# Kernel optimization log

Hardware: AMD Instinct MI355X
Metric: run time of the kernel (lower is better)

The kernel has to match this reference:

```python
import jax, jax.numpy as jnp
import numpy as np
import math

B, S, H, D = 1, 2048, 12, 128
DIM = H * D
BLKQ, BLKK = 128, 64
TOPK = 0.2
EPS = 1e-6
NEG = -1e30


def setup_inputs() -> dict:
    key = jax.random.key(0)
    ks = jax.random.split(key, 8)
    hidden_states = jax.random.normal(ks[0], (B, S, DIM), jnp.float32)
    # interleaved RoPE tables: even slots hold cos, odd slots hold sin phase copies
    pos = np.arange(S, dtype=np.float64)[:, None]
    inv = 1.0 / (10000.0 ** (np.arange(0, D, 2, dtype=np.float64) / D))
    ang = pos * inv[None, :]                       # [S, D/2]
    freqs_cos = jnp.asarray(np.repeat(np.cos(ang), 2, axis=-1), jnp.float32).reshape(1, S, 1, D)
    freqs_sin = jnp.asarray(np.repeat(np.sin(ang), 2, axis=-1), jnp.float32).reshape(1, S, 1, D)
    sc = 1.0 / math.sqrt(DIM)
    Wq = jax.random.normal(ks[1], (DIM, DIM), jnp.float32) * sc
    Wk = jax.random.normal(ks[2], (DIM, DIM), jnp.float32) * sc
    Wv = jax.random.normal(ks[3], (DIM, DIM), jnp.float32) * sc
    Wo = jax.random.normal(ks[4], (DIM, DIM), jnp.float32) * sc
    bq = jax.random.normal(ks[5], (DIM,), jnp.float32) * 0.01
    bk = jax.random.normal(ks[6], (DIM,), jnp.float32) * 0.01
    bv = jax.random.normal(ks[7], (DIM,), jnp.float32) * 0.01
    bo = jnp.zeros((DIM,), jnp.float32)
    gq = jnp.ones((DIM,), jnp.float32)
    gk = jnp.ones((DIM,), jnp.float32)
    return dict(hidden_states=hidden_states, freqs_cos=freqs_cos, freqs_sin=freqs_sin,
                Wq=Wq, bq=bq, Wk=Wk, bk=bk, Wv=Wv, bv=bv, Wo=Wo, bo=bo, gq=gq, gk=gk)


def _rmsnorm(x, g):
    return x * jax.lax.rsqrt(jnp.mean(x * x, axis=-1, keepdims=True) + EPS) * g


def _rope(x, fc, fs):
    # x: [B,S,H,D]; interleaved even/odd rotation as in _apply_rotary_emb
    x1 = x[..., 0::2]
    x2 = x[..., 1::2]
    cos = fc[..., 0::2]
    sin = fs[..., 1::2]
    even = x1 * cos - x2 * sin
    odd = x1 * sin + x2 * cos
    return jnp.stack([even, odd], axis=-1).reshape(x.shape)


def _sla(q, k, v):
    # q,k,v: [B,H,S,D]. Top-k block-sparse exact attention + linear attention
    # (softmax feature map) on the unselected blocks, jointly normalized.
    nqb, nkb = S // BLKQ, S // BLKK
    ksel = max(1, int(math.ceil(TOPK * nkb)))
    qb = q.reshape(B, H, nqb, BLKQ, D).mean(axis=3)
    kb = k.reshape(B, H, nkb, BLKK, D).mean(axis=3)
    blk_scores = jnp.einsum('bhqd,bhkd->bhqk', qb, kb)
    _, idx = jax.lax.top_k(blk_scores, ksel)                  # [B,H,nqb,ksel]
    bmask = (jax.nn.one_hot(idx, nkb, dtype=jnp.float32).sum(axis=-2) > 0)
    mask = jnp.repeat(jnp.repeat(bmask, BLKQ, axis=2), BLKK, axis=3)  # [B,H,S,S]

    scale = 1.0 / math.sqrt(D)
    s = jnp.einsum('bhqd,bhkd->bhqk', q, k) * scale
    m = jnp.max(jnp.where(mask, s, NEG), axis=-1, keepdims=True)
    p = jnp.where(mask, jnp.exp(s - m), 0.0)
    num_s = jnp.einsum('bhqk,bhkd->bhqd', p, v)
    den_s = p.sum(axis=-1, keepdims=True)

    lq = jax.nn.softmax(q, axis=-1)
    lk = jax.nn.softmax(k, axis=-1)
    L = jnp.where(mask, 0.0, jnp.einsum('bhqd,bhkd->bhqk', lq, lk))
    num_l = jnp.einsum('bhqk,bhkd->bhqd', L, v)
    den_l = L.sum(axis=-1, keepdims=True)

    w = jnp.exp(-m)  # bring linear part onto the max-shifted exp scale
    return (num_s + w * num_l) / (den_s + w * den_l)


def reference(hidden_states, freqs_cos, freqs_sin, Wq, bq, Wk, bk, Wv, bv, Wo, bo, gq, gk):
    q = _rmsnorm(hidden_states @ Wq + bq, gq).reshape(B, S, H, D)
    k = _rmsnorm(hidden_states @ Wk + bk, gk).reshape(B, S, H, D)
    v = (hidden_states @ Wv + bv).reshape(B, S, H, D)
    q = _rope(q, freqs_cos, freqs_sin)
    k = _rope(k, freqs_cos, freqs_sin)
    q, k, v = (t.transpose(0, 2, 1, 3) for t in (q, k, v))  # [B,H,S,D]
    o = _sla(q, k, v)
    o = o.transpose(0, 2, 1, 3).reshape(B, S, DIM)
    return o @ Wo + bo
```

## Files before the change

### kernel.cpp

```cpp
#include <hip/hip_runtime.h>
#include <hip/hip_bf16.h>

#define SQ   2048
#define DIMM 1536
#define QS   4608
#define NH   12
#define DH   128
#define NQB  16
#define NKB  32
#define KSEL 7

typedef unsigned short u16;
typedef __bf16 bf16x8 __attribute__((ext_vector_type(8)));
typedef _Float16 f16x8 __attribute__((ext_vector_type(8)));
typedef short  s16x8  __attribute__((ext_vector_type(8)));
typedef float  f32x4  __attribute__((ext_vector_type(4)));
typedef u16    u16x4  __attribute__((ext_vector_type(4)));

__device__ __forceinline__ float bf2f(u16 u) {
  unsigned int x = ((unsigned int)u) << 16;
  return __builtin_bit_cast(float, x);
}
__device__ __forceinline__ u16 f2bf(float f) {
  unsigned int x = __builtin_bit_cast(unsigned int, f);
  x += 0x7fffu + ((x >> 16) & 1u);
  return (u16)(x >> 16);
}

typedef __attribute__((address_space(3))) void lds_vt;
typedef const __attribute__((address_space(1))) void g_vt;
__device__ __forceinline__ void dma16(const void* g, void* l) {
  __builtin_amdgcn_global_load_lds((g_vt*)g, (lds_vt*)l, 16, 0, 0);
}

__global__ __launch_bounds__(256) void prep_all(const float* __restrict__ hs,
                                                u16* __restrict__ hh,
                                                u16* __restrict__ hl,
                                                const float* __restrict__ W0,
                                                const float* __restrict__ W1,
                                                const float* __restrict__ W2,
                                                const float* __restrict__ W3,
                                                u16* __restrict__ WTh,
                                                u16* __restrict__ WTl) {
  __shared__ float tile[64][65];
  int bx = blockIdx.x;
  if (bx < 1536) {
    size_t i = ((size_t)bx * 256 + threadIdx.x) * 8;
    f32x4 a = *(const f32x4*)&hs[i];
    f32x4 b = *(const f32x4*)&hs[i + 4];
    s16x8 h, l;
    #pragma unroll
    for (int j = 0; j < 4; j++) {
      u16 hj = f2bf(a[j]); h[j] = (short)hj; l[j] = (short)f2bf(a[j] - bf2f(hj));
      u16 hk = f2bf(b[j]); h[4 + j] = (short)hk; l[4 + j] = (short)f2bf(b[j] - bf2f(hk));
    }
    *(s16x8*)&hh[i] = h;
    *(s16x8*)&hl[i] = l;
    return;
  }
  int b2 = bx - 1536;
  int wi = b2 / 576;
  int rest = b2 % 576;
  int k0 = (rest / 24) * 64, n0 = (rest % 24) * 64;
  const float* W = (wi == 0) ? W0 : (wi == 1) ? W1 : (wi == 2) ? W2 : W3;
  int x = threadIdx.x & 63, y = threadIdx.x >> 6;
  #pragma unroll
  for (int i = 0; i < 16; i++) {
    int k = y + i * 4;
    tile[k][x] = W[(size_t)(k0 + k) * DIMM + n0 + x];
  }
  __syncthreads();
  size_t obase = (size_t)wi * DIMM * DIMM;
  #pragma unroll
  for (int rep = 0; rep < 2; rep++) {
    int u = threadIdx.x + rep * 256;
    int n = u >> 3, c8 = u & 7;
    s16x8 hv, lv;
    #pragma unroll
    for (int e = 0; e < 8; e++) {
      float v = tile[c8 * 8 + e][n];
      if (wi == 3) {
        hv[e] = (short)__builtin_bit_cast(u16, (_Float16)v);
      } else {
        u16 hb = f2bf(v);
        hv[e] = (short)hb;
        lv[e] = (short)f2bf(v - bf2f(hb));
      }
    }
    size_t oi = obase + (size_t)(n0 + n) * DIMM + k0 + c8 * 8;
    *(s16x8*)&WTh[oi] = hv;
    if (wi != 3) *(s16x8*)&WTl[oi] = lv;
  }
}

__global__ __launch_bounds__(512, 4) void gemm3_k(const u16* __restrict__ Ahp,
                                                  const u16* __restrict__ Alp,
                                                  const u16* __restrict__ WTh,
                                                  const u16* __restrict__ WTl,
                                                  const float* __restrict__ bq,
                                                  const float* __restrict__ bk,
                                                  const float* __restrict__ bv,
                                                  float* __restrict__ C,
                                                  u16* __restrict__ vbfT) {
  __shared__ u16 As[2][128][64];
  __shared__ u16 Bs[2][128][64];
  const int tid = threadIdx.x;
  const int w = tid >> 6, lane = tid & 63, quad = lane >> 4, l16 = lane & 15;
  const int wr = w >> 2, wc = w & 3;
  const int m_base = blockIdx.y * 128;
  const int nt = blockIdx.x;
  const int wi = nt / 12;
  const int n_in = (nt % 12) * 128;
  const u16* Bh0 = WTh + ((size_t)wi * DIMM + n_in) * DIMM;
  const u16* Bl0 = WTl + ((size_t)wi * DIMM + n_in) * DIMM;
  const float* bias = (wi == 0) ? bq : (wi == 1) ? bk : bv;
  const bool split = (wi != 2);

  const int srow = lane >> 3;
  const int skc = (((lane & 7) ^ srow) * 8);
  const int rx = (l16 & 7);

  f32x4 zero4 = {0.f, 0.f, 0.f, 0.f};
  f32x4 acc[4][2];
  #pragma unroll
  for (int i = 0; i < 4; i++)
    #pragma unroll
    for (int j = 0; j < 2; j++) acc[i][j] = zero4;

  for (int k0 = 0; k0 < DIMM; k0 += 64) {
    #pragma unroll
    for (int c = 0; c < 2; c++) {
      int r0 = w * 16 + c * 8;
      int row = r0 + srow;
      dma16(&Ahp[(size_t)(m_base + row) * DIMM + k0 + skc], &As[0][r0][0]);
      dma16(&Bh0[(size_t)row * DIMM + k0 + skc], &Bs[0][r0][0]);
      if (split) {
        dma16(&Alp[(size_t)(m_base + row) * DIMM + k0 + skc], &As[1][r0][0]);
        dma16(&Bl0[(size_t)row * DIMM + k0 + skc], &Bs[1][r0][0]);
      }
    }
    __syncthreads();
    #pragma unroll
    for (int kk = 0; kk < 2; kk++) {
      const int coff = ((kk * 4 + quad) ^ rx) * 8;
      bf16x8 afh[4], afl[4], bfh[2], bfl[2];
      #pragma unroll
      for (int i = 0; i < 4; i++)
        afh[i] = __builtin_bit_cast(bf16x8,
                 *(const s16x8*)&As[0][wr * 64 + i * 16 + l16][coff]);
      #pragma unroll
      for (int j = 0; j < 2; j++)
        bfh[j] = __builtin_bit_cast(bf16x8,
                 *(const s16x8*)&Bs[0][wc * 32 + j * 16 + l16][coff]);
      if (split) {
        #pragma unroll
        for (int i = 0; i < 4; i++)
          afl[i] = __builtin_bit_cast(bf16x8,
                   *(const s16x8*)&As[1][wr * 64 + i * 16 + l16][coff]);
        #pragma unroll
        for (int j = 0; j < 2; j++)
          bfl[j] = __builtin_bit_cast(bf16x8,
                   *(const s16x8*)&Bs[1][wc * 32 + j * 16 + l16][coff]);
      }
      #pragma unroll
      for (int i = 0; i < 4; i++)
        #pragma unroll
        for (int j = 0; j < 2; j++) {
          acc[i][j] = __builtin_amdgcn_mfma_f32_16x16x32_bf16(afh[i], bfh[j], acc[i][j], 0, 0, 0);
          if (split) {
            acc[i][j] = __builtin_amdgcn_mfma_f32_16x16x32_bf16(afh[i], bfl[j], acc[i][j], 0, 0, 0);
            acc[i][j] = __builtin_amdgcn_mfma_f32_16x16x32_bf16(afl[i], bfh[j], acc[i][j], 0, 0, 0);
          }
        }
    }
    __syncthreads();
  }

  if (wi != 2) {
    #pragma unroll
    for (int i = 0; i < 4; i++)
      #pragma unroll
      for (int j = 0; j < 2; j++) {
        int tc = wc * 32 + j * 16 + l16;
        float bv2 = bias[n_in + tc];
        #pragma unroll
        for (int rg = 0; rg < 4; rg++) {
          int r = m_base + wr * 64 + i * 16 + quad * 4 + rg;
          C[(size_t)r * QS + nt * 128 + tc] = acc[i][j][rg] + bv2;
        }
      }
  } else {
    int hh = nt % 12;
    int bblk = blockIdx.y * 2 + wr;
    u16* vb = vbfT + (size_t)(hh * NKB + bblk) * 8192;
    int kb8 = quad >> 1;
    int klo = (quad & 1) * 4;
    #pragma unroll
    for (int i = 0; i < 4; i++) {
      int k8 = (i * 2 + kb8);
      #pragma unroll
      for (int j = 0; j < 2; j++) {
        int d = wc * 32 + j * 16 + l16;
        float bv2 = bias[n_in + d];
        u16x4 o;
        #pragma unroll
        for (int rg = 0; rg < 4; rg++) o[rg] = f2bf(acc[i][j][rg] + bv2);
        *(u16x4*)&vb[d * 64 + ((k8 ^ (d & 7)) << 3) + klo] = o;
      }
    }
  }
}

__global__ __launch_bounds__(256) void gemm_o(const u16* __restrict__ Ap,
                                              const u16* __restrict__ Bp,
                                              const float* __restrict__ bias,
                                              float* __restrict__ C) {
  __shared__ u16 As[64][64];
  __shared__ u16 Bs[128][64];
  const int tid = threadIdx.x;
  const int w = tid >> 6, lane = tid & 63, quad = lane >> 4, l16 = lane & 15;
  const int wr = w >> 1, wc = w & 1;
  const int m_base = blockIdx.y * 64, n_base = blockIdx.x * 128;
  const int srow = lane >> 3;
  const int skc = (((lane & 7) ^ srow) * 8);
  const int rx = (l16 & 7);

  f32x4 zero4 = {0.f, 0.f, 0.f, 0.f};
  f32x4 acc[2][4];
  #pragma unroll
  for (int i = 0; i < 2; i++)
    #pragma unroll
    for (int j = 0; j < 4; j++) acc[i][j] = zero4;

  for (int k0 = 0; k0 < DIMM; k0 += 64) {
    #pragma unroll
    for (int c = 0; c < 2; c++) {
      int r0 = w * 16 + c * 8;
      int row = r0 + srow;
      dma16(&Ap[(size_t)(m_base + row) * DIMM + k0 + skc], &As[r0][0]);
    }
    #pragma unroll
    for (int c = 0; c < 4; c++) {
      int r0 = w * 32 + c * 8;
      int row = r0 + srow;
      dma16(&Bp[(size_t)(n_base + row) * DIMM + k0 + skc], &Bs[r0][0]);
    }
    __syncthreads();
    #pragma unroll
    for (int kk = 0; kk < 2; kk++) {
      const int coff = ((kk * 4 + quad) ^ rx) * 8;
      f16x8 af[2], bf[4];
      #pragma unroll
      for (int i = 0; i < 2; i++)
        af[i] = __builtin_bit_cast(f16x8,
                *(const s16x8*)&As[wr * 32 + i * 16 + l16][coff]);
      #pragma unroll
      for (int j = 0; j < 4; j++)
        bf[j] = __builtin_bit_cast(f16x8,
                *(const s16x8*)&Bs[wc * 64 + j * 16 + l16][coff]);
      #pragma unroll
      for (int i = 0; i < 2; i++)
        #pragma unroll
        for (int j = 0; j < 4; j++)
          acc[i][j] = __builtin_amdgcn_mfma_f32_16x16x32_f16(af[i], bf[j], acc[i][j], 0, 0, 0);
    }
    __syncthreads();
  }
  #pragma unroll
  for (int i = 0; i < 2; i++)
    #pragma unroll
    for (int j = 0; j < 4; j++) {
      int c = n_base + wc * 64 + j * 16 + l16;
      float bv2 = bias[c];
      #pragma unroll
      for (int rg = 0; rg < 4; rg++) {
        int r = m_base + wr * 32 + i * 16 + quad * 4 + rg;
        C[(size_t)r * DIMM + c] = acc[i][j][rg] + bv2;
      }
    }
}

__global__ __launch_bounds__(256) void norm_rope_k(float* __restrict__ qkv,
                                                   const float* __restrict__ gq,
                                                   const float* __restrict__ gk,
                                                   const float* __restrict__ fc,
                                                   const float* __restrict__ fs,
                                                   u16* __restrict__ qbf,
                                                   u16* __restrict__ kbf) {
  int s = blockIdx.x;
  float* row = qkv + (size_t)s * QS + (blockIdx.y == 0 ? 0 : DIMM);
  const float* g = (blockIdx.y == 0) ? gq : gk;
  u16* obase = (blockIdx.y == 0) ? qbf : kbf;
  int t = threadIdx.x;
  float ss = 0.f;
  #pragma unroll
  for (int i = 0; i < 6; i++) {
    float v = row[t + i * 256];
    ss += v * v;
  }
  #pragma unroll
  for (int m = 1; m < 64; m <<= 1) ss += __shfl_xor(ss, m, 64);
  __shared__ float wsum[4];
  if ((t & 63) == 0) wsum[t >> 6] = ss;
  __syncthreads();
  float tot = wsum[0] + wsum[1] + wsum[2] + wsum[3];
  float sc = rsqrtf(tot / 1536.0f + 1e-6f);
  #pragma unroll
  for (int i = 0; i < 3; i++) {
    int p = t + i * 256;
    int h = p >> 6, ip = p & 63;
    int base = h * 128 + 2 * ip;
    float x1 = row[base] * sc * g[base];
    float x2 = row[base + 1] * sc * g[base + 1];
    float c = fc[(size_t)s * 128 + 2 * ip];
    float sn = fs[(size_t)s * 128 + 2 * ip + 1];
    float ev = x1 * c - x2 * sn;
    float od = x1 * sn + x2 * c;
    row[base]     = ev;
    row[base + 1] = od;
    int gsk = ip >> 2, e = (2 * ip) & 7;
    int cc = (gsk & 8) | ((gsk ^ (s & 7)) & 7);
    u16* ob = obase + ((size_t)h * SQ + s) * 128;
    unsigned int pack = (unsigned int)f2bf(ev) | ((unsigned int)f2bf(od) << 16);
    *(unsigned int*)&ob[cc * 8 + e] = pack;
  }
}

__global__ __launch_bounds__(256) void kvmeans_k(const float* __restrict__ qf,
                                                 const float* __restrict__ kf,
                                                 const u16* __restrict__ vbfT,
                                                 float* __restrict__ KV,
                                                 float* __restrict__ slk,
                                                 float* __restrict__ qb,
                                                 float* __restrict__ kb) {
  __shared__ u16 lkT[128 * 72];
  __shared__ u16 vtT[128 * 64];
  int h = blockIdx.y, t = threadIdx.x;
  if (blockIdx.x >= NKB) {
    int mx = blockIdx.x - NKB;
    if (t < 128) {
      if (mx < NQB) {
        float a = 0.f;
        for (int r = 0; r < 128; r++) a += qf[(size_t)(mx * 128 + r) * QS + h * DH + t];
        qb[(h * NQB + mx) * DH + t] = a * (1.0f / 128.0f);
      } else {
        int ki = mx - NQB;
        float a = 0.f;
        for (int r = 0; r < 64; r++) a += kf[(size_t)(ki * 64 + r) * QS + h * DH + t];
        kb[(h * NKB + ki) * DH + t] = a * (1.0f / 64.0f);
      }
    }
    return;
  }
  int kbi = blockIdx.x;
  int w = t >> 6, lane = t & 63, quad = lane >> 4, l16 = lane & 15;

  {
    const u16* vsrc = vbfT + ((size_t)(h * NKB + kbi)) * 128 * 64;
    #pragma unroll
    for (int c = 0; c < 4; c++)
      dma16(vsrc + (w * 32 + c * 8) * 64 + lane * 8, &vtT[(w * 32 + c * 8) * 64]);
  }
  {
    int r = t >> 2, q4 = t & 3;
    const float* kr = kf + (size_t)(kbi * 64 + r) * QS + h * DH;
    f32x4 x[8];
    float mx = -3.4e38f;
    #pragma unroll
    for (int i = 0; i < 8; i++) {
      x[i] = *(const f32x4*)&kr[q4 * 32 + i * 4];
      mx = fmaxf(mx, fmaxf(fmaxf(x[i][0], x[i][1]), fmaxf(x[i][2], x[i][3])));
    }
    mx = fmaxf(mx, __shfl_xor(mx, 1, 64));
    mx = fmaxf(mx, __shfl_xor(mx, 2, 64));
    float sum = 0.f;
    #pragma unroll
    for (int i = 0; i < 8; i++)
      #pragma unroll
      for (int e = 0; e < 4; e++) { float v = __expf(x[i][e] - mx); x[i][e] = v; sum += v; }
    sum += __shfl_xor(sum, 1, 64);
    sum += __shfl_xor(sum, 2, 64);
    float inv = 1.0f / sum;
    #pragma unroll
    for (int i = 0; i < 8; i++)
      #pragma unroll
      for (int e = 0; e < 4; e++)
        lkT[(q4 * 32 + i * 4 + e) * 72 + r] = f2bf(x[i][e] * inv);
  }
  __syncthreads();

  f32x4 zero4 = {0.f, 0.f, 0.f, 0.f};
  f32x4 acc[2][8];
  #pragma unroll
  for (int i = 0; i < 2; i++)
    #pragma unroll
    for (int j = 0; j < 8; j++) acc[i][j] = zero4;
  #pragma unroll
  for (int kk = 0; kk < 2; kk++) {
    bf16x8 af[2];
    #pragma unroll
    for (int i = 0; i < 2; i++)
      af[i] = __builtin_bit_cast(bf16x8,
              *(const s16x8*)&lkT[(w * 32 + i * 16 + l16) * 72 + kk * 32 + quad * 8]);
    const int voff = ((kk * 4 + quad) ^ (l16 & 7)) * 8;
    #pragma unroll
    for (int j = 0; j < 8; j++) {
      bf16x8 vb = __builtin_bit_cast(bf16x8, *(const s16x8*)&vtT[(j * 16 + l16) * 64 + voff]);
      #pragma unroll
      for (int i = 0; i < 2; i++)
        acc[i][j] = __builtin_amdgcn_mfma_f32_16x16x32_bf16(af[i], vb, acc[i][j], 0, 0, 0);
    }
  }
  float* out = KV + (size_t)(h * NKB + kbi) * 16384;
  #pragma unroll
  for (int i = 0; i < 2; i++)
    #pragma unroll
    for (int j = 0; j < 8; j++) {
      #pragma unroll
      for (int rg = 0; rg < 4; rg++) {
        int r = w * 32 + i * 16 + quad * 4 + rg;
        int c = j * 16 + l16;
        out[(size_t)r * 128 + c] = acc[i][j][rg];
      }
    }
  if (t < 128) {
    float a = 0.f;
    #pragma unroll
    for (int c8 = 0; c8 < 8; c8++) {
      s16x8 v8 = *(const s16x8*)&lkT[t * 72 + c8 * 8];
      #pragma unroll
      for (int e = 0; e < 8; e++) a += bf2f((u16)v8[e]);
    }
    slk[(h * NKB + kbi) * DH + t] = a;
  }
}

__global__ __launch_bounds__(256) void kvtot_topk_k(const float* __restrict__ KV,
                                                    const float* __restrict__ slk,
                                                    const float* __restrict__ qb,
                                                    const float* __restrict__ kb,
                                                    float* __restrict__ KVtot,
                                                    float* __restrict__ sltot,
                                                    int* __restrict__ sel) {
  int h = blockIdx.y, t = threadIdx.x;
  if (blockIdx.x < 64) {
    int e = blockIdx.x * 256 + t;
    float a = 0.f;
    for (int b = 0; b < NKB; b++) a += KV[(size_t)(h * NKB + b) * 16384 + e];
    KVtot[(size_t)h * 16384 + e] = a;
    if (blockIdx.x == 0 && t < 128) {
      float s2 = 0.f;
      for (int b = 0; b < NKB; b++) s2 += slk[(h * NKB + b) * DH + t];
      sltot[h * DH + t] = s2;
    }
    return;
  }
  int qi = blockIdx.x - 64;
  __shared__ float scs[NKB];
  int r = t >> 3, sub = t & 7;
  const float* qv = qb + (size_t)(h * NQB + qi) * DH;
  const float* kv2 = kb + (size_t)(h * NKB + r) * DH;
  float a = 0.f;
  #pragma unroll
  for (int dd = 0; dd < 16; dd++) a += qv[sub * 16 + dd] * kv2[sub * 16 + dd];
  a += __shfl_xor(a, 1, 64);
  a += __shfl_xor(a, 2, 64);
  a += __shfl_xor(a, 4, 64);
  if (sub == 0) scs[r] = a;
  __syncthreads();
  if (t == 0) {
    unsigned int used = 0;
    for (int it = 0; it < KSEL; it++) {
      float best = -3.4e38f; int bi = 0;
      for (int j = 0; j < NKB; j++)
        if (!((used >> j) & 1) && scs[j] > best) { best = scs[j]; bi = j; }
      used |= 1u << bi;
      sel[(h * NQB + qi) * 8 + it] = bi;
    }
  }
}

__global__ __launch_bounds__(256) void attn_k(const u16* __restrict__ qbf,
                                              const u16* __restrict__ kbf,
                                              const u16* __restrict__ vbfT,
                                              const int* __restrict__ sel,
                                              const float* __restrict__ KV,
                                              const float* __restrict__ slk,
                                              const float* __restrict__ KVtot,
                                              const float* __restrict__ sltot,
                                              u16* __restrict__ of16) {
  __shared__ u16 smem[25600];
  __shared__ float mrow[64], lrow[64], dent[64], slsh[128];
  __shared__ int selsh[KSEL];
  u16* qt  = smem;
  u16* vtT = smem + 8192;
  u16* kt  = smem + 16384;
  u16* ptb = smem + 16384;
  u16* MT  = smem + 8192;

  int h = blockIdx.y, qi = blockIdx.x, tid = threadIdx.x;
  int w = tid >> 6, lane = tid & 63, quad = lane >> 4, l16 = lane & 15;

  {
    const u16* qsrc = qbf + ((size_t)h * SQ + qi * 64) * 128;
    #pragma unroll
    for (int c = 0; c < 4; c++)
      dma16(qsrc + (w * 16 + c * 4) * 128 + lane * 8, &qt[(w * 16 + c * 4) * 128]);
  }
  if (tid < KSEL) selsh[tid] = sel[(h * NQB + (qi >> 1)) * 8 + tid];
  __syncthreads();

  float m_run[4], l_run[4];
  f32x4 zero4 = {0.f, 0.f, 0.f, 0.f};
  f32x4 oacc[8];
  #pragma unroll
  for (int rg = 0; rg < 4; rg++) { m_run[rg] = -3.0e38f; l_run[rg] = 0.f; }
  #pragma unroll
  for (int nt = 0; nt < 8; nt++) oacc[nt] = zero4;

  for (int bi = 0; bi < KSEL; bi++) {
    int b = selsh[bi];
    {
      const u16* ksrc = kbf + ((size_t)h * SQ + b * 64) * 128;
      #pragma unroll
      for (int c = 0; c < 4; c++)
        dma16(ksrc + (w * 16 + c * 4) * 128 + lane * 8, &kt[(w * 16 + c * 4) * 128]);
      const u16* vsrc = vbfT + ((size_t)(h * NKB + b)) * 128 * 64;
      #pragma unroll
      for (int c = 0; c < 4; c++)
        dma16(vsrc + (w * 32 + c * 8) * 64 + lane * 8, &vtT[(w * 32 + c * 8) * 64]);
    }
    __syncthreads();

    f32x4 sacc[4];
    #pragma unroll
    for (int nt = 0; nt < 4; nt++) sacc[nt] = zero4;
    __builtin_amdgcn_s_setprio(1);
    #pragma unroll
    for (int kk = 0; kk < 4; kk++) {
      const int kkq = kk * 4 + quad;
      const int qoff = ((kkq & 8) | ((kkq ^ (l16 & 7)) & 7)) * 8;
      bf16x8 af = __builtin_bit_cast(bf16x8, *(const s16x8*)&qt[(w * 16 + l16) * 128 + qoff]);
      #pragma unroll
      for (int nt = 0; nt < 4; nt++) {
        bf16x8 bfr = __builtin_bit_cast(bf16x8, *(const s16x8*)&kt[(nt * 16 + l16) * 128 + qoff]);
        sacc[nt] = __builtin_amdgcn_mfma_f32_16x16x32_bf16(af, bfr, sacc[nt], 0, 0, 0);
      }
    }
    __builtin_amdgcn_s_setprio(0);
    const float SCALE = 0.08838834764831845f;
    #pragma unroll
    for (int nt = 0; nt < 4; nt++) sacc[nt] *= SCALE;

    #pragma unroll
    for (int rg = 0; rg < 4; rg++) {
      float bmax = fmaxf(fmaxf(sacc[0][rg], sacc[1][rg]),
                         fmaxf(sacc[2][rg], sacc[3][rg]));
      bmax = fmaxf(bmax, __shfl_xor(bmax, 1, 64));
      bmax = fmaxf(bmax, __shfl_xor(bmax, 2, 64));
      bmax = fmaxf(bmax, __shfl_xor(bmax, 4, 64));
      bmax = fmaxf(bmax, __shfl_xor(bmax, 8, 64));
      float mold = m_run[rg];
      float mnew = fmaxf(mold, bmax);
      float alpha = __expf(mold - mnew);
      float rs = 0.f;
      #pragma unroll
      for (int nt = 0; nt < 4; nt++) {
        float p = __expf(sacc[nt][rg] - mnew);
        sacc[nt][rg] = p; rs += p;
      }
      rs += __shfl_xor(rs, 1, 64);
      rs += __shfl_xor(rs, 2, 64);
      rs += __shfl_xor(rs, 4, 64);
      rs += __shfl_xor(rs, 8, 64);
      m_run[rg] = mnew;
      l_run[rg] = l_run[rg] * alpha + rs;
      #pragma unroll
      for (int nt = 0; nt < 8; nt++) oacc[nt][rg] *= alpha;
    }
    __syncthreads();
    #pragma unroll
    for (int rg = 0; rg < 4; rg++) {
      int r = w * 16 + quad * 4 + rg;
      #pragma unroll
      for (int nt = 0; nt < 4; nt++) ptb[r * 72 + nt * 16 + l16] = f2bf(sacc[nt][rg]);
    }
    __syncthreads();

    __builtin_amdgcn_s_setprio(1);
    #pragma unroll
    for (int kk = 0; kk < 2; kk++) {
      bf16x8 pa = __builtin_bit_cast(bf16x8, *(const s16x8*)&ptb[(w * 16 + l16) * 72 + kk * 32 + quad * 8]);
      #pragma unroll
      for (int nt = 0; nt < 8; nt++) {
        const int voff = ((kk * 4 + quad) ^ (l16 & 7)) * 8;
        bf16x8 vb = __builtin_bit_cast(bf16x8, *(const s16x8*)&vtT[(nt * 16 + l16) * 64 + voff]);
        oacc[nt] = __builtin_amdgcn_mfma_f32_16x16x32_bf16(pa, vb, oacc[nt], 0, 0, 0);
      }
    }
    __builtin_amdgcn_s_setprio(0);
    __syncthreads();
  }

  if (l16 == 0) {
    #pragma unroll
    for (int rg = 0; rg < 4; rg++) {
      int r = w * 16 + quad * 4 + rg;
      mrow[r] = m_run[rg];
      lrow[r] = l_run[rg];
    }
  }
  if (tid < 128) {
    float a = sltot[h * DH + tid];
    #pragma unroll
    for (int i = 0; i < KSEL; i++) a -= slk[(h * NKB + selsh[i]) * DH + tid];
    slsh[tid] = a;
  }
  for (int i = 0; i < 16; i++) {
    int idx = i * 256 + tid;
    int e4 = idx * 4;
    int d1 = e4 >> 7, d2 = e4 & 127;
    f32x4 a = *(const f32x4*)&KVtot[(size_t)h * 16384 + e4];
    #pragma unroll
    for (int k2 = 0; k2 < KSEL; k2++) {
      f32x4 s4 = *(const f32x4*)&KV[(size_t)(h * NKB + selsh[k2]) * 16384 + e4];
      a -= s4;
    }
    #pragma unroll
    for (int j = 0; j < 4; j++) MT[(d2 + j) * 136 + d1] = f2bf(a[j]);
  }
  __syncthreads();

  {
    int r = tid >> 2, sub = tid & 3;
    float w_r = __expf(-mrow[r]);
    float mx = -3.4e38f;
    #pragma unroll
    for (int gi = 0; gi < 4; gi++) {
      int gc = sub * 4 + gi;
      int c = (gc & 8) | ((gc ^ (r & 7)) & 7);
      #pragma unroll
      for (int e = 0; e < 8; e++) mx = fmaxf(mx, bf2f(qt[r * 128 + c * 8 + e]));
    }
    mx = fmaxf(mx, __shfl_xor(mx, 1, 64));
    mx = fmaxf(mx, __shfl_xor(mx, 2, 64));
    float sum = 0.f;
    #pragma unroll
    for (int gi = 0; gi < 4; gi++) {
      int gc = sub * 4 + gi;
      int c = (gc & 8) | ((gc ^ (r & 7)) & 7);
      #pragma unroll
      for (int e = 0; e < 8; e++) sum += __expf(bf2f(qt[r * 128 + c * 8 + e]) - mx);
    }
    sum += __shfl_xor(sum, 1, 64);
    sum += __shfl_xor(sum, 2, 64);
    float sc2 = w_r / sum;
    float dl = 0.f;
    #pragma unroll
    for (int gi = 0; gi < 4; gi++) {
      int gc = sub * 4 + gi;
      int c = (gc & 8) | ((gc ^ (r & 7)) & 7);
      #pragma unroll
      for (int e = 0; e < 8; e++) {
        float lq = __expf(bf2f(qt[r * 128 + c * 8 + e]) - mx) * sc2;
        dl += lq * slsh[gc * 8 + e];
        qt[r * 128 + c * 8 + e] = f2bf(lq);
      }
    }
    dl += __shfl_xor(dl, 1, 64);
    dl += __shfl_xor(dl, 2, 64);
    if (sub == 0) dent[r] = lrow[r] + dl;
  }
  __syncthreads();

  __builtin_amdgcn_s_setprio(1);
  #pragma unroll
  for (int kk = 0; kk < 4; kk++) {
    const int kkq = kk * 4 + quad;
    const int qoff = ((kkq & 8) | ((kkq ^ (l16 & 7)) & 7)) * 8;
    bf16x8 af = __builtin_bit_cast(bf16x8, *(const s16x8*)&qt[(w * 16 + l16) * 128 + qoff]);
    #pragma unroll
    for (int nt = 0; nt < 8; nt++) {
      bf16x8 mb = __builtin_bit_cast(bf16x8, *(const s16x8*)&MT[(nt * 16 + l16) * 136 + kk * 32 + quad * 8]);
      oacc[nt] = __builtin_amdgcn_mfma_f32_16x16x32_bf16(af, mb, oacc[nt], 0, 0, 0);
    }
  }
  __builtin_amdgcn_s_setprio(0);

  #pragma unroll
  for (int rg = 0; rg < 4; rg++) {
    int r = w * 16 + quad * 4 + rg;
    float inv = 1.0f / dent[r];
    #pragma unroll
    for (int nt = 0; nt < 8; nt++) {
      int c = nt * 16 + l16;
      float v = oacc[nt][rg] * inv;
      size_t oi = (size_t)(qi * 64 + r) * DIMM + h * DH + c;
      of16[oi] = __builtin_bit_cast(u16, (_Float16)v);
    }
  }
}

extern "C" void kernel_launch(void* const* d_in, const int* in_sizes, int n_in,
                              void* d_out, int out_size, void* d_ws, size_t ws_size,
                              hipStream_t stream) {
  const float* hs = (const float*)d_in[0];
  const float* fc = (const float*)d_in[1];
  const float* fs = (const float*)d_in[2];
  const float* Wq = (const float*)d_in[3];
  const float* bq = (const float*)d_in[4];
  const float* Wk = (const float*)d_in[5];
  const float* bk = (const float*)d_in[6];
  const float* Wv = (const float*)d_in[7];
  const float* bv = (const float*)d_in[8];
  const float* Wo = (const float*)d_in[9];
  const float* bo = (const float*)d_in[10];
  const float* gq = (const float*)d_in[11];
  const float* gk = (const float*)d_in[12];

  char* p = (char*)d_ws;
  auto alloc = [&](size_t bytes) {
    char* r = p; p += (bytes + 255) & ~(size_t)255; return r;
  };
  u16* WTh = (u16*)alloc((size_t)4 * DIMM * DIMM * 2);
  u16* WTl = (u16*)alloc((size_t)4 * DIMM * DIMM * 2);
  u16* hsh = (u16*)alloc((size_t)SQ * DIMM * 2);
  u16* hsl = (u16*)alloc((size_t)SQ * DIMM * 2);
  float* qkv = (float*)alloc((size_t)SQ * QS * 4);
  u16* qbf = (u16*)alloc((size_t)NH * SQ * DH * 2);
  u16* kbf = (u16*)alloc((size_t)NH * SQ * DH * 2);
  u16* vbfT = (u16*)alloc((size_t)NH * NKB * DH * 64 * 2);
  float* qb = (float*)alloc((size_t)NH * NQB * DH * 4);
  float* kb = (float*)alloc((size_t)NH * NKB * DH * 4);
  int* sel = (int*)alloc((size_t)NH * NQB * 8 * 4);
  float* KV = (float*)alloc((size_t)NH * NKB * DH * DH * 4);
  float* slk = (float*)alloc((size_t)NH * NKB * DH * 4);
  float* KVtot = (float*)alloc((size_t)NH * DH * DH * 4);
  float* sltot = (float*)alloc((size_t)NH * DH * 4);

  float* qf = qkv;
  float* kf = qkv + DIMM;

  prep_all<<<1536 + 2304, 256, 0, stream>>>(hs, hsh, hsl, Wq, Wk, Wv, Wo, WTh, WTl);

  gemm3_k<<<dim3(36, 16), 512, 0, stream>>>(hsh, hsl, WTh, WTl, bq, bk, bv, qkv, vbfT);

  norm_rope_k<<<dim3(SQ, 2), 256, 0, stream>>>(qkv, gq, gk, fc, fs, qbf, kbf);
  kvmeans_k<<<dim3(NKB + NQB + NKB, NH), 256, 0, stream>>>(qf, kf, vbfT, KV, slk, qb, kb);
  kvtot_topk_k<<<dim3(64 + NQB, NH), 256, 0, stream>>>(KV, slk, qb, kb, KVtot, sltot, sel);

  u16* of16 = hsh;
  attn_k<<<dim3(2 * NQB, NH), 256, 0, stream>>>(qbf, kbf, vbfT, sel, KV, slk, KVtot, sltot, of16);

  const u16* WTo = WTh + (size_t)3 * DIMM * DIMM;
  gemm_o<<<dim3(12, 32), 256, 0, stream>>>(of16, WTo, bo, (float*)d_out);
}
```

Before: 306.8 us.

## Double-buffer QKV GEMM K-loop and precompute linear-attention MT per query block

The QKV GEMM now splits each 64-wide K step into two 32-wide halves held in separate LDS buffers, issuing the DMA for the next half while MFMAs run on the current one. This hides global load latency inside the K loop. Separately, a new mt_k kernel builds the bf16 transposed KV-minus-selected matrix once per query block and writes it pre-swizzled to global memory. attn_k then loads it with DMA instead of recomputing it, removing redundant fp32 reductions that were done twice per query block. This adds a kernel launch and extra global traffic, and reuses the hsl buffer as scratch.

```diff
diff --git a/kernel.cpp b/kernel.cpp
--- a/kernel.cpp
+++ b/kernel.cpp
@@ -102,8 +102,8 @@
                                                   const float* __restrict__ bv,
                                                   float* __restrict__ C,
                                                   u16* __restrict__ vbfT) {
-  __shared__ u16 As[2][128][64];
-  __shared__ u16 Bs[2][128][64];
+  __shared__ u16 As[2][2][128][32];
+  __shared__ u16 Bs[2][2][128][32];
   const int tid = threadIdx.x;
   const int w = tid >> 6, lane = tid & 63, quad = lane >> 4, l16 = lane & 15;
   const int wr = w >> 2, wc = w & 3;
@@ -116,9 +116,11 @@
   const float* bias = (wi == 0) ? bq : (wi == 1) ? bk : bv;
   const bool split = (wi != 2);
 
-  const int srow = lane >> 3;
-  const int skc = (((lane & 7) ^ srow) * 8);
-  const int rx = (l16 & 7);
+  const int srow = lane >> 2;
+  const int skc = (((lane & 3) ^ (srow & 3)) * 8);
+  const int r0s = w * 16;
+  const size_t aoff = (size_t)(m_base + r0s + srow) * DIMM + skc;
+  const size_t boff = (size_t)(r0s + srow) * DIMM + skc;
 
   f32x4 zero4 = {0.f, 0.f, 0.f, 0.f};
   f32x4 acc[4][2];
@@ -127,52 +129,55 @@
     #pragma unroll
     for (int j = 0; j < 2; j++) acc[i][j] = zero4;
 
-  for (int k0 = 0; k0 < DIMM; k0 += 64) {
-    #pragma unroll
-    for (int c = 0; c < 2; c++) {
-      int r0 = w * 16 + c * 8;
-      int row = r0 + srow;
-      dma16(&Ahp[(size_t)(m_base + row) * DIMM + k0 + skc], &As[0][r0][0]);
-      dma16(&Bh0[(size_t)row * DIMM + k0 + skc], &Bs[0][r0][0]);
-      if (split) {
-        dma16(&Alp[(size_t)(m_base + row) * DIMM + k0 + skc], &As[1][r0][0]);
-        dma16(&Bl0[(size_t)row * DIMM + k0 + skc], &Bs[1][r0][0]);
-      }
-    }
+  auto stage = [&](int b, int k0) {
+    dma16(&Ahp[aoff + k0], &As[b][0][r0s][0]);
+    dma16(&Bh0[boff + k0], &Bs[b][0][r0s][0]);
+    if (split) {
+      dma16(&Alp[aoff + k0], &As[b][1][r0s][0]);
+      dma16(&Bl0[boff + k0], &Bs[b][1][r0s][0]);
+    }
+  };
+  const int coff = (quad ^ (l16 & 3)) * 8;
+  auto compute = [&](int b) {
+    bf16x8 afh[4], afl[4], bfh[2], bfl[2];
+    #pragma unroll
+    for (int i = 0; i < 4; i++)
+      afh[i] = __builtin_bit_cast(bf16x8,
+               *(const s16x8*)&As[b][0][wr * 64 + i * 16 + l16][coff]);
+    #pragma unroll
+    for (int j = 0; j < 2; j++)
+      bfh[j] = __builtin_bit_cast(bf16x8,
+               *(const s16x8*)&Bs[b][0][wc * 32 + j * 16 + l16][coff]);
+    if (split) {
+      #pragma unroll
+      for (int i = 0; i < 4; i++)
+        afl[i] = __builtin_bit_cast(bf16x8,
+                 *(const s16x8*)&As[b][1][wr * 64 + i * 16 + l16][coff]);
+      #pragma unroll
+      for (int j = 0; j < 2; j++)
+        bfl[j] = __builtin_bit_cast(bf16x8,
+                 *(const s16x8*)&Bs[b][1][wc * 32 + j * 16 + l16][coff]);
+    }
+    #pragma unroll
+    for (int i = 0; i < 4; i++)
+      #pragma unroll
+      for (int j = 0; j < 2; j++) {
+        acc[i][j] = __builtin_amdgcn_mfma_f32_16x16x32_bf16(afh[i], bfh[j], acc[i][j], 0, 0, 0);
+        if (split) {
+          acc[i][j] = __builtin_amdgcn_mfma_f32_16x16x32_bf16(afh[i], bfl[j], acc[i][j], 0, 0, 0);
+          acc[i][j] = __builtin_amdgcn_mfma_f32_16x16x32_bf16(afl[i], bfh[j], acc[i][j], 0, 0, 0);
+        }
+      }
+  };
+
+  stage(0, 0);
+  __syncthreads();
+  for (int step = 0; step < 24; step++) {
+    stage(1, step * 64 + 32);
+    compute(0);
     __syncthreads();
-    #pragma unroll
-    for (int kk = 0; kk < 2; kk++) {
-      const int coff = ((kk * 4 + quad) ^ rx) * 8;
-      bf16x8 afh[4], afl[4], bfh[2], bfl[2];
-      #pragma unroll
-      for (int i = 0; i < 4; i++)
-        afh[i] = __builtin_bit_cast(bf16x8,
-                 *(const s16x8*)&As[0][wr * 64 + i * 16 + l16][coff]);
-      #pragma unroll
-      for (int j = 0; j < 2; j++)
-        bfh[j] = __builtin_bit_cast(bf16x8,
-                 *(const s16x8*)&Bs[0][wc * 32 + j * 16 + l16][coff]);
-      if (split) {
-        #pragma unroll
-        for (int i = 0; i < 4; i++)
-          afl[i] = __builtin_bit_cast(bf16x8,
-                   *(const s16x8*)&As[1][wr * 64 + i * 16 + l16][coff]);
-        #pragma unroll
-        for (int j = 0; j < 2; j++)
-          bfl[j] = __builtin_bit_cast(bf16x8,
-                   *(const s16x8*)&Bs[1][wc * 32 + j * 16 + l16][coff]);
-      }
-      #pragma unroll
-      for (int i = 0; i < 4; i++)
-        #pragma unroll
-        for (int j = 0; j < 2; j++) {
-          acc[i][j] = __builtin_amdgcn_mfma_f32_16x16x32_bf16(afh[i], bfh[j], acc[i][j], 0, 0, 0);
-          if (split) {
-            acc[i][j] = __builtin_amdgcn_mfma_f32_16x16x32_bf16(afh[i], bfl[j], acc[i][j], 0, 0, 0);
-            acc[i][j] = __builtin_amdgcn_mfma_f32_16x16x32_bf16(afl[i], bfh[j], acc[i][j], 0, 0, 0);
-          }
-        }
-    }
+    if (step < 23) stage(0, step * 64 + 64);
+    compute(1);
     __syncthreads();
   }
 
@@ -480,14 +485,46 @@
   }
 }
 
+__global__ __launch_bounds__(256) void mt_k(const int* __restrict__ sel,
+                                            const float* __restrict__ KV,
+                                            const float* __restrict__ KVtot,
+                                            u16* __restrict__ MTg) {
+  __shared__ u16 MT[128 * 136];
+  __shared__ int selsh[KSEL];
+  int h = blockIdx.y, q2 = blockIdx.x, tid = threadIdx.x;
+  if (tid < KSEL) selsh[tid] = sel[(h * NQB + q2) * 8 + tid];
+  __syncthreads();
+  for (int i = 0; i < 16; i++) {
+    int idx = i * 256 + tid;
+    int e4 = idx * 4;
+    int d1 = e4 >> 7, d2 = e4 & 127;
+    f32x4 a = *(const f32x4*)&KVtot[(size_t)h * 16384 + e4];
+    #pragma unroll
+    for (int k2 = 0; k2 < KSEL; k2++) {
+      f32x4 s4 = *(const f32x4*)&KV[(size_t)(h * NKB + selsh[k2]) * 16384 + e4];
+      a -= s4;
+    }
+    #pragma unroll
+    for (int j = 0; j < 4; j++) MT[(d2 + j) * 136 + d1] = f2bf(a[j]);
+  }
+  __syncthreads();
+  u16* out = MTg + (size_t)(h * NQB + q2) * 16384;
+  #pragma unroll
+  for (int i = 0; i < 8; i++) {
+    int u = i * 256 + tid;
+    int r = u >> 4, kc = u & 15;
+    int sc = (kc & 8) | ((kc ^ (r & 7)) & 7);
+    *(s16x8*)&out[r * 128 + sc * 8] = *(const s16x8*)&MT[r * 136 + kc * 8];
+  }
+}
+
 __global__ __launch_bounds__(256) void attn_k(const u16* __restrict__ qbf,
                                               const u16* __restrict__ kbf,
                                               const u16* __restrict__ vbfT,
                                               const int* __restrict__ sel,
-                                              const float* __restrict__ KV,
                                               const float* __restrict__ slk,
-                                              const float* __restrict__ KVtot,
                                               const float* __restrict__ sltot,
+                                              const u16* __restrict__ MTg,
                                               u16* __restrict__ of16) {
   __shared__ u16 smem[25600];
   __shared__ float mrow[64], lrow[64], dent[64], slsh[128];
@@ -602,6 +639,12 @@
     __syncthreads();
   }
 
+  {
+    const u16* mtb = MTg + (size_t)(h * NQB + (qi >> 1)) * 16384;
+    #pragma unroll
+    for (int c = 0; c < 8; c++)
+      dma16(mtb + (w * 32 + c * 4) * 128 + lane * 8, &MT[(w * 32 + c * 4) * 128]);
+  }
   if (l16 == 0) {
     #pragma unroll
     for (int rg = 0; rg < 4; rg++) {
@@ -616,19 +659,6 @@
     for (int i = 0; i < KSEL; i++) a -= slk[(h * NKB + selsh[i]) * DH + tid];
     slsh[tid] = a;
   }
-  for (int i = 0; i < 16; i++) {
-    int idx = i * 256 + tid;
-    int e4 = idx * 4;
-    int d1 = e4 >> 7, d2 = e4 & 127;
-    f32x4 a = *(const f32x4*)&KVtot[(size_t)h * 16384 + e4];
-    #pragma unroll
-    for (int k2 = 0; k2 < KSEL; k2++) {
-      f32x4 s4 = *(const f32x4*)&KV[(size_t)(h * NKB + selsh[k2]) * 16384 + e4];
-      a -= s4;
-    }
-    #pragma unroll
-    for (int j = 0; j < 4; j++) MT[(d2 + j) * 136 + d1] = f2bf(a[j]);
-  }
   __syncthreads();
 
   {
@@ -681,7 +711,9 @@
     bf16x8 af = __builtin_bit_cast(bf16x8, *(const s16x8*)&qt[(w * 16 + l16) * 128 + qoff]);
     #pragma unroll
     for (int nt = 0; nt < 8; nt++) {
-      bf16x8 mb = __builtin_bit_cast(bf16x8, *(const s16x8*)&MT[(nt * 16 + l16) * 136 + kk * 32 + quad * 8]);
+      const int kc = kk * 4 + quad;
+      const int mo = ((kc & 8) | ((kc ^ (l16 & 7)) & 7)) * 8;
+      bf16x8 mb = __builtin_bit_cast(bf16x8, *(const s16x8*)&MT[(nt * 16 + l16) * 128 + mo]);
       oacc[nt] = __builtin_amdgcn_mfma_f32_16x16x32_bf16(af, mb, oacc[nt], 0, 0, 0);
     }
   }
@@ -750,7 +782,9 @@
   kvtot_topk_k<<<dim3(64 + NQB, NH), 256, 0, stream>>>(KV, slk, qb, kb, KVtot, sltot, sel);
 
   u16* of16 = hsh;
-  attn_k<<<dim3(2 * NQB, NH), 256, 0, stream>>>(qbf, kbf, vbfT, sel, KV, slk, KVtot, sltot, of16);
+  u16* MTg = hsl;
+  mt_k<<<dim3(NQB, NH), 256, 0, stream>>>(sel, KV, KVtot, MTg);
+  attn_k<<<dim3(2 * NQB, NH), 256, 0, stream>>>(qbf, kbf, vbfT, sel, slk, sltot, MTg, of16);
 
   const u16* WTo = WTh + (size_t)3 * DIMM * DIMM;
   gemm_o<<<dim3(12, 32), 256, 0, stream>>>(of16, WTo, bo, (float*)d_out);
```

Result: slower. 316.1 us (+3.0%).

## Precompute linear-attention KV matrix per query-block pair in a separate kernel

Applied to the files above, without the earlier changes.

Moves the KVtot-minus-selected-blocks reduction out of attn_k into a new mt_k kernel. It runs once per query block of 128 and writes a swizzled bf16 matrix to global memory, so the two 64-row attention blocks that share a selection no longer each redo the 8 float loads per element. attn_k then fetches the ready matrix with DMA loads, uses separate shared-memory regions for K, V and P, and drops two barriers in the inner loop. This costs an extra kernel launch, a global write and read of the bf16 matrix, and more shared memory per block.

```diff
diff --git a/kernel.cpp b/kernel.cpp
--- a/kernel.cpp
+++ b/kernel.cpp
@@ -480,22 +480,54 @@
   }
 }
 
+__global__ __launch_bounds__(256) void mt_k(const int* __restrict__ sel,
+                                            const float* __restrict__ KV,
+                                            const float* __restrict__ KVtot,
+                                            u16* __restrict__ MTg) {
+  __shared__ u16 MT[128 * 136];
+  __shared__ int selsh[KSEL];
+  int h = blockIdx.y, q2 = blockIdx.x, tid = threadIdx.x;
+  if (tid < KSEL) selsh[tid] = sel[(h * NQB + q2) * 8 + tid];
+  __syncthreads();
+  for (int i = 0; i < 16; i++) {
+    int idx = i * 256 + tid;
+    int e4 = idx * 4;
+    int d1 = e4 >> 7, d2 = e4 & 127;
+    f32x4 a = *(const f32x4*)&KVtot[(size_t)h * 16384 + e4];
+    #pragma unroll
+    for (int k2 = 0; k2 < KSEL; k2++) {
+      f32x4 s4 = *(const f32x4*)&KV[(size_t)(h * NKB + selsh[k2]) * 16384 + e4];
+      a -= s4;
+    }
+    #pragma unroll
+    for (int j = 0; j < 4; j++) MT[(d2 + j) * 136 + d1] = f2bf(a[j]);
+  }
+  __syncthreads();
+  u16* out = MTg + (size_t)(h * NQB + q2) * 16384;
+  #pragma unroll
+  for (int i = 0; i < 8; i++) {
+    int u = i * 256 + tid;
+    int r = u >> 4, kc = u & 15;
+    int sc = (kc & 8) | ((kc ^ (r & 7)) & 7);
+    *(s16x8*)&out[r * 128 + sc * 8] = *(const s16x8*)&MT[r * 136 + kc * 8];
+  }
+}
+
 __global__ __launch_bounds__(256) void attn_k(const u16* __restrict__ qbf,
                                               const u16* __restrict__ kbf,
                                               const u16* __restrict__ vbfT,
                                               const int* __restrict__ sel,
-                                              const float* __restrict__ KV,
                                               const float* __restrict__ slk,
-                                              const float* __restrict__ KVtot,
                                               const float* __restrict__ sltot,
+                                              const u16* __restrict__ MTg,
                                               u16* __restrict__ of16) {
-  __shared__ u16 smem[25600];
+  __shared__ u16 smem[29184];
   __shared__ float mrow[64], lrow[64], dent[64], slsh[128];
   __shared__ int selsh[KSEL];
   u16* qt  = smem;
-  u16* vtT = smem + 8192;
-  u16* kt  = smem + 16384;
-  u16* ptb = smem + 16384;
+  u16* kt  = smem + 8192;
+  u16* vtT = smem + 16384;
+  u16* ptb = smem + 24576;
   u16* MT  = smem + 8192;
 
   int h = blockIdx.y, qi = blockIdx.x, tid = threadIdx.x;
@@ -578,14 +610,12 @@
       #pragma unroll
       for (int nt = 0; nt < 8; nt++) oacc[nt][rg] *= alpha;
     }
-    __syncthreads();
     #pragma unroll
     for (int rg = 0; rg < 4; rg++) {
       int r = w * 16 + quad * 4 + rg;
       #pragma unroll
       for (int nt = 0; nt < 4; nt++) ptb[r * 72 + nt * 16 + l16] = f2bf(sacc[nt][rg]);
     }
-    __syncthreads();
 
     __builtin_amdgcn_s_setprio(1);
     #pragma unroll
@@ -602,6 +632,12 @@
     __syncthreads();
   }
 
+  {
+    const u16* mtb = MTg + (size_t)(h * NQB + (qi >> 1)) * 16384;
+    #pragma unroll
+    for (int c = 0; c < 8; c++)
+      dma16(mtb + (w * 32 + c * 4) * 128 + lane * 8, &MT[(w * 32 + c * 4) * 128]);
+  }
   if (l16 == 0) {
     #pragma unroll
     for (int rg = 0; rg < 4; rg++) {
@@ -616,19 +652,6 @@
     for (int i = 0; i < KSEL; i++) a -= slk[(h * NKB + selsh[i]) * DH + tid];
     slsh[tid] = a;
   }
-  for (int i = 0; i < 16; i++) {
-    int idx = i * 256 + tid;
-    int e4 = idx * 4;
-    int d1 = e4 >> 7, d2 = e4 & 127;
-    f32x4 a = *(const f32x4*)&KVtot[(size_t)h * 16384 + e4];
-    #pragma unroll
-    for (int k2 = 0; k2 < KSEL; k2++) {
-      f32x4 s4 = *(const f32x4*)&KV[(size_t)(h * NKB + selsh[k2]) * 16384 + e4];
-      a -= s4;
-    }
-    #pragma unroll
-    for (int j = 0; j < 4; j++) MT[(d2 + j) * 136 + d1] = f2bf(a[j]);
-  }
   __syncthreads();
 
   {
@@ -681,7 +704,9 @@
     bf16x8 af = __builtin_bit_cast(bf16x8, *(const s16x8*)&qt[(w * 16 + l16) * 128 + qoff]);
     #pragma unroll
     for (int nt = 0; nt < 8; nt++) {
-      bf16x8 mb = __builtin_bit_cast(bf16x8, *(const s16x8*)&MT[(nt * 16 + l16) * 136 + kk * 32 + quad * 8]);
+      const int kc = kk * 4 + quad;
+      const int mo = ((kc & 8) | ((kc ^ (l16 & 7)) & 7)) * 8;
+      bf16x8 mb = __builtin_bit_cast(bf16x8, *(const s16x8*)&MT[(nt * 16 + l16) * 128 + mo]);
       oacc[nt] = __builtin_amdgcn_mfma_f32_16x16x32_bf16(af, mb, oacc[nt], 0, 0, 0);
     }
   }
@@ -750,7 +775,9 @@
   kvtot_topk_k<<<dim3(64 + NQB, NH), 256, 0, stream>>>(KV, slk, qb, kb, KVtot, sltot, sel);
 
   u16* of16 = hsh;
-  attn_k<<<dim3(2 * NQB, NH), 256, 0, stream>>>(qbf, kbf, vbfT, sel, KV, slk, KVtot, sltot, of16);
+  u16* MTg = hsl;
+  mt_k<<<dim3(NQB, NH), 256, 0, stream>>>(sel, KV, KVtot, MTg);
+  attn_k<<<dim3(2 * NQB, NH), 256, 0, stream>>>(qbf, kbf, vbfT, sel, slk, sltot, MTg, of16);
 
   const u16* WTo = WTh + (size_t)3 * DIMM * DIMM;
   gemm_o<<<dim3(12, 32), 256, 0, stream>>>(of16, WTo, bo, (float*)d_out);
```

Measured after the change: 308.3 us. No clear change (+0.5%).
